# Kernel tuning notes

Measured on AMD Instinct MI355X. Metric: run time of the kernel, lower is better.

Reference implementation:

```python
import jax, jax.numpy as jnp
import numpy as np

ALPHA = 0.2  # LeakyReLU negative slope
NEG_INF = -9e15


def setup_inputs() -> dict:
    key = jax.random.key(0)
    ks = jax.random.split(key, 6)
    B, N, F_in, F_out = 16, 1024, 1024, 512
    x = jax.random.normal(ks[0], (B, N, F_in), dtype=jnp.float32)
    adj = jax.random.randint(ks[1], (B, N, N), 0, 2, dtype=jnp.int32)
    W = jax.random.normal(ks[2], (F_in, F_out), dtype=jnp.float32) * 0.02
    a = jax.random.normal(ks[3], (2 * F_out, 1), dtype=jnp.float32) * 0.02
    fc_w = jax.random.normal(ks[4], (F_out, 2 * F_out), dtype=jnp.float32) * 0.02
    fc_b = jnp.zeros((F_out,), dtype=jnp.float32)
    return {"x": x, "adj": adj, "W": W, "a": a, "fc_w": fc_w, "fc_b": fc_b}


def reference(x, adj, W, a, fc_w, fc_b):
    # h: [B, N, F_out]
    h = jnp.matmul(x, W)
    F_out = W.shape[1]
    # The original builds a_input = concat(h_i, h_j) of shape [B,N,N,2F] and
    # contracts with a. Equivalently (same math, no O(N^2 F) intermediate):
    # e_ij = leakyrelu(h_i . a[:F] + h_j . a[F:])
    a1 = a[:F_out, 0]  # [F_out]
    a2 = a[F_out:, 0]  # [F_out]
    f1 = jnp.einsum('bnf,f->bn', h, a1)  # source term
    f2 = jnp.einsum('bnf,f->bn', h, a2)  # target term
    e = jax.nn.leaky_relu(f1[:, :, None] + f2[:, None, :], negative_slope=ALPHA)  # [B,N,N]
    attention = jnp.where(adj > 0, e, jnp.full_like(e, NEG_INF))
    attention = jax.nn.softmax(attention, axis=2)
    # dropout is identity in eval mode
    agg = jnp.matmul(attention, h)  # [B,N,F_out]
    h_prime = jnp.concatenate([agg, h], axis=2)  # [B,N,2F]
    h_prime = jnp.matmul(h_prime, fc_w.T) + fc_b
    return jax.nn.elu(h_prime)  # concat=True path
```

## Files before the change

### kernel.cpp

```cpp
#include <hip/hip_runtime.h>

#define ALPHA 0.2f

typedef __attribute__((ext_vector_type(8))) short short8;
typedef __attribute__((ext_vector_type(4))) float f32x4;

__device__ __forceinline__ unsigned short f2b(float f) {
  unsigned int u; __builtin_memcpy(&u, &f, 4);
  unsigned int r = (u + 0x7FFFu + ((u >> 16) & 1u)) >> 16;
  return (unsigned short)r;
}
__device__ __forceinline__ float b2f(unsigned short v) {
  unsigned int u = ((unsigned int)v) << 16; float f; __builtin_memcpy(&f, &u, 4); return f;
}
__device__ __forceinline__ void gl_lds16(const unsigned short* g, unsigned short* l) {
  __builtin_amdgcn_global_load_lds((__attribute__((address_space(1))) void*)g,
                                   (__attribute__((address_space(3))) void*)l, 16, 0, 0);
}

__device__ __forceinline__ void cvt8(const float* __restrict__ in, unsigned short* __restrict__ out,
                                     unsigned int gid) {
  float4 v0 = ((const float4*)in)[gid * 2];
  float4 v1 = ((const float4*)in)[gid * 2 + 1];
  alignas(16) unsigned short o[8];
  o[0] = f2b(v0.x); o[1] = f2b(v0.y); o[2] = f2b(v0.z); o[3] = f2b(v0.w);
  o[4] = f2b(v1.x); o[5] = f2b(v1.y); o[6] = f2b(v1.z); o[7] = f2b(v1.w);
  ((uint4*)out)[gid] = *(const uint4*)o;
}

__global__ __launch_bounds__(256) void prep1(const int* __restrict__ adj,
                                             unsigned short* __restrict__ bm16,
                                             const float* __restrict__ x,
                                             unsigned short* __restrict__ xb,
                                             const float* __restrict__ fcw,
                                             unsigned short* __restrict__ fcwb,
                                             const float* __restrict__ W,
                                             unsigned short* __restrict__ Wt) {
  __shared__ alignas(16) unsigned short tile[64][72];
  unsigned int bx = blockIdx.x;
  unsigned int tid = threadIdx.x;
  if (bx < 4096u) {
    unsigned int gid = bx * 256 + tid;
    const int4* a4 = (const int4*)adj;
    int4 v0 = a4[gid * 4 + 0];
    int4 v1 = a4[gid * 4 + 1];
    int4 v2 = a4[gid * 4 + 2];
    int4 v3 = a4[gid * 4 + 3];
    unsigned int bits = 0;
    bits |= (v0.x > 0) << 0;  bits |= (v0.y > 0) << 1;  bits |= (v0.z > 0) << 2;  bits |= (v0.w > 0) << 3;
    bits |= (v1.x > 0) << 4;  bits |= (v1.y > 0) << 5;  bits |= (v1.z > 0) << 6;  bits |= (v1.w > 0) << 7;
    bits |= (v2.x > 0) << 8;  bits |= (v2.y > 0) << 9;  bits |= (v2.z > 0) << 10; bits |= (v2.w > 0) << 11;
    bits |= (v3.x > 0) << 12; bits |= (v3.y > 0) << 13; bits |= (v3.z > 0) << 14; bits |= (v3.w > 0) << 15;
    bm16[gid] = (unsigned short)bits;
  } else if (bx < 12288u) {
    cvt8(x, xb, (bx - 4096u) * 256 + tid);
  } else if (bx < 12544u) {
    cvt8(fcw, fcwb, (bx - 12288u) * 256 + tid);
  } else {
    unsigned int idx = bx - 12544u;
    unsigned int k0 = (idx >> 3) * 64, n0 = (idx & 7) * 64;
    #pragma unroll
    for (int p = 0; p < 4; p++) {
      int r = p * 16 + (tid >> 4);
      int c = (tid & 15) * 4;
      float4 v = *(const float4*)(W + (size_t)(k0 + r) * 512 + n0 + c);
      tile[r][c] = f2b(v.x); tile[r][c + 1] = f2b(v.y);
      tile[r][c + 2] = f2b(v.z); tile[r][c + 3] = f2b(v.w);
    }
    __syncthreads();
    int f = tid >> 2;
    int ic = (tid & 3) * 16;
    alignas(16) unsigned short buf[16];
    #pragma unroll
    for (int k = 0; k < 16; k++) buf[k] = tile[ic + k][f];
    uint4* dst = (uint4*)(Wt + (size_t)(n0 + f) * 1024 + k0 + ic);
    dst[0] = ((const uint4*)buf)[0];
    dst[1] = ((const uint4*)buf)[1];
  }
}

__global__ __launch_bounds__(256) void prep2(const unsigned short* __restrict__ hp,
                                             const float* __restrict__ a,
                                             float* __restrict__ f1, float* __restrict__ f2,
                                             unsigned short* __restrict__ ht) {
  __shared__ alignas(16) unsigned short tile[64][72];
  int bx = blockIdx.x;
  int tid = threadIdx.x;
  if (bx < 4096) {
    int row = bx * 4 + (tid >> 6);
    int lane = tid & 63;
    const unsigned short* hrow = hp + (size_t)row * 1024 + 512;
    uint4 raw = *(const uint4*)(hrow + lane * 8);
    alignas(16) unsigned short hv[8]; __builtin_memcpy(hv, &raw, 16);
    float s1 = 0.f, s2 = 0.f;
    #pragma unroll
    for (int j = 0; j < 8; j++) {
      float hf = b2f(hv[j]);
      s1 += hf * a[lane * 8 + j];
      s2 += hf * a[512 + lane * 8 + j];
    }
    #pragma unroll
    for (int o = 32; o > 0; o >>= 1) { s1 += __shfl_down(s1, o); s2 += __shfl_down(s2, o); }
    if (lane == 0) { f1[row] = s1; f2[row] = s2; }
  } else {
    int idx = bx - 4096;
    int b = idx >> 7;
    int f0 = ((idx >> 4) & 7) * 64;
    int i0 = (idx & 15) * 64;
    #pragma unroll
    for (int p = 0; p < 2; p++) {
      int r = p * 32 + (tid >> 3);
      int c = (tid & 7) * 8;
      uint4 v = *(const uint4*)(hp + (size_t)(b * 1024 + i0 + r) * 1024 + 512 + f0 + c);
      *(uint4*)(&tile[r][c]) = v;
    }
    __syncthreads();
    int f = tid >> 2;
    int ic = (tid & 3) * 16;
    alignas(16) unsigned short buf[16];
    #pragma unroll
    for (int k = 0; k < 16; k++) buf[k] = tile[ic + k][f];
    uint4* dst = (uint4*)(ht + (size_t)(b * 512 + f0 + f) * 1024 + i0 + ic);
    dst[0] = ((const uint4*)buf)[0];
    dst[1] = ((const uint4*)buf)[1];
  }
}

__global__ __launch_bounds__(256) void rowsum_P(const unsigned short* __restrict__ bm16,
                                                const float* __restrict__ f1,
                                                const float* __restrict__ f2,
                                                float* __restrict__ invl,
                                                unsigned short* __restrict__ P) {
  int row = blockIdx.x * 4 + (threadIdx.x >> 6);
  int lane = threadIdx.x & 63;
  int b = row >> 10;
  float f1v = f1[row];
  unsigned int bits = bm16[(size_t)row * 64 + lane];
  const float* f2p = f2 + (b << 10) + lane * 16;
  float4 v0 = ((const float4*)f2p)[0];
  float4 v1 = ((const float4*)f2p)[1];
  float4 v2 = ((const float4*)f2p)[2];
  float4 v3 = ((const float4*)f2p)[3];
  float fv[16] = {v0.x, v0.y, v0.z, v0.w, v1.x, v1.y, v1.z, v1.w,
                  v2.x, v2.y, v2.z, v2.w, v3.x, v3.y, v3.z, v3.w};
  float s = 0.f;
  alignas(16) unsigned short o[16];
  #pragma unroll
  for (int j = 0; j < 16; j++) {
    float p = 0.f;
    if ((bits >> j) & 1u) {
      float z = f1v + fv[j];
      z = z > 0.f ? z : ALPHA * z;
      p = __expf(z);
      s += p;
    }
    o[j] = f2b(p);
  }
  uint4* dst = (uint4*)(P + (size_t)row * 1024 + lane * 16);
  dst[0] = ((const uint4*)o)[0];
  dst[1] = ((const uint4*)o)[1];
  #pragma unroll
  for (int off = 32; off > 0; off >>= 1) s += __shfl_down(s, off);
  if (lane == 0) invl[row] = 1.0f / s;
}

template <int EPI>
__global__ __launch_bounds__(256) void gemm_bt(
    const unsigned short* __restrict__ A, size_t aBS,
    const unsigned short* __restrict__ Bt, size_t bBS,
    int K,
    void* __restrict__ outp, size_t oBS, int ldo, int ocol,
    const float* __restrict__ scale,
    const float* __restrict__ bias) {
  __shared__ alignas(16) unsigned short As[128 * 64];
  __shared__ alignas(16) unsigned short Bs[128 * 64];
  const int tid = threadIdx.x;
  const int lane = tid & 63;
  const int w = tid >> 6;
  const int m0 = blockIdx.x * 128;
  const int n0 = blockIdx.y * 128;
  const int zb = blockIdx.z;
  const unsigned short* Ab = A + (size_t)zb * aBS;
  const unsigned short* Btb = Bt + (size_t)zb * bBS;

  f32x4 acc[4][4];
  #pragma unroll
  for (int i = 0; i < 4; i++)
    #pragma unroll
    for (int j = 0; j < 4; j++)
      #pragma unroll
      for (int r = 0; r < 4; r++) acc[i][j][r] = 0.f;

  const int lr = lane >> 3;
  const int lc = (lane & 7) ^ (lr & 7);
  const unsigned short* ag = Ab + (size_t)(m0 + w * 32 + lr) * K + lc * 8;
  const unsigned short* bg = Btb + (size_t)(n0 + w * 32 + lr) * K + lc * 8;
  unsigned short* asl = As + w * 32 * 64;
  unsigned short* bsl = Bs + w * 32 * 64;

  const int wm = (w & 1) * 64;
  const int wn = (w >> 1) * 64;
  const int row16 = lane & 15;
  const int quad = lane >> 4;
  const int sw = row16 & 7;

  for (int k0 = 0; k0 < K; k0 += 64) {
    __syncthreads();
    #pragma unroll
    for (int t = 0; t < 4; t++) {
      gl_lds16(ag + k0 + (size_t)(t * 8) * K, asl + t * 512);
      gl_lds16(bg + k0 + (size_t)(t * 8) * K, bsl + t * 512);
    }
    __syncthreads();
    short8 af[2][4], bf[2][4];
    #pragma unroll
    for (int s = 0; s < 2; s++) {
      #pragma unroll
      for (int i = 0; i < 4; i++) {
        af[s][i] = *(const short8*)(As + (wm + i * 16 + row16) * 64 + ((s * 4 + quad) ^ sw) * 8);
        bf[s][i] = *(const short8*)(Bs + (wn + i * 16 + row16) * 64 + ((s * 4 + quad) ^ sw) * 8);
      }
    }
    #pragma unroll
    for (int s = 0; s < 2; s++)
      #pragma unroll
      for (int am = 0; am < 4; am++)
        #pragma unroll
        for (int bn = 0; bn < 4; bn++)
          acc[am][bn] = __builtin_amdgcn_mfma_f32_16x16x32_bf16(af[s][am], bf[s][bn], acc[am][bn], 0, 0, 0);
  }

  const int col = lane & 15;
  const int r0 = quad * 4;
  #pragma unroll
  for (int am = 0; am < 4; am++) {
    #pragma unroll
    for (int bn = 0; bn < 4; bn++) {
      #pragma unroll
      for (int r = 0; r < 4; r++) {
        int m = m0 + wm + am * 16 + r0 + r;
        int n = n0 + wn + bn * 16 + col;
        float v = acc[am][bn][r];
        if (EPI == 3) v *= scale[zb * 1024 + m];
        if (EPI == 2) {
          v += bias[n];
          v = v > 0.f ? v : expm1f(v);
          ((float*)outp)[(size_t)m * ldo + n] = v;
        } else {
          ((unsigned short*)outp)[(size_t)zb * oBS + (size_t)m * ldo + ocol + n] = f2b(v);
        }
      }
    }
  }
}

extern "C" void kernel_launch(void* const* d_in, const int* in_sizes, int n_in,
                              void* d_out, int out_size, void* d_ws, size_t ws_size,
                              hipStream_t stream) {
  const float* x   = (const float*)d_in[0];
  const int*   adj = (const int*)d_in[1];
  const float* W   = (const float*)d_in[2];
  const float* a   = (const float*)d_in[3];
  const float* fcw = (const float*)d_in[4];
  const float* fcb = (const float*)d_in[5];
  float* out = (float*)d_out;
  char* ws = (char*)d_ws;

  unsigned short* xb   = (unsigned short*)(ws);
  unsigned short* hp   = (unsigned short*)(ws + 33554432);
  unsigned short* ht   = (unsigned short*)(ws + 67108864);
  unsigned short* Wt   = (unsigned short*)(ws + 83886080);
  unsigned short* fcwb = (unsigned short*)(ws + 84934656);
  float* f1            = (float*)(ws + 85983232);
  float* f2            = (float*)(ws + 86048768);
  float* invl          = (float*)(ws + 86114304);
  unsigned short* bm   = (unsigned short*)(ws + 86179840);
  unsigned short* P = xb;

  prep1<<<12672, 256, 0, stream>>>(adj, bm, x, xb, fcw, fcwb, W, Wt);

  gemm_bt<1><<<dim3(128, 4, 1), 256, 0, stream>>>(xb, 0, Wt, 0, 1024,
                                                  hp, 0, 1024, 512, nullptr, nullptr);
  prep2<<<6144, 256, 0, stream>>>(hp, a, f1, f2, ht);
  rowsum_P<<<4096, 256, 0, stream>>>(bm, f1, f2, invl, P);

  gemm_bt<3><<<dim3(8, 4, 16), 256, 0, stream>>>(P, 1024 * 1024, ht, 512 * 1024, 1024,
                                                 hp, 1024 * 1024, 1024, 0, invl, nullptr);
  gemm_bt<2><<<dim3(128, 4, 1), 256, 0, stream>>>(hp, 0, fcwb, 0, 1024,
                                                  out, 0, 512, 0, nullptr, fcb);
}
```

Measured before the change: 265.8 us.

## Double-buffer GEMM LDS tiles and coalesce adjacency and conversion prep loads

The bf16 GEMM now uses two LDS buffers per operand and issues the next K-tile's global-to-LDS loads before computing on the current tile, with one barrier per iteration instead of two. The goal is to overlap global memory latency with MFMA work. In the prep kernel, adjacency bitmask packing and fp32-to-bf16 conversion are reorganized for coalesced per-lane 16-byte loads, using shuffles to assemble the mask bits. The cost is double the LDS per block (64KB), which may lower occupancy.

```diff
diff --git a/kernel.cpp b/kernel.cpp
--- a/kernel.cpp
+++ b/kernel.cpp
@@ -18,14 +18,13 @@
                                    (__attribute__((address_space(3))) void*)l, 16, 0, 0);
 }
 
-__device__ __forceinline__ void cvt8(const float* __restrict__ in, unsigned short* __restrict__ out,
-                                     unsigned int gid) {
-  float4 v0 = ((const float4*)in)[gid * 2];
-  float4 v1 = ((const float4*)in)[gid * 2 + 1];
-  alignas(16) unsigned short o[8];
-  o[0] = f2b(v0.x); o[1] = f2b(v0.y); o[2] = f2b(v0.z); o[3] = f2b(v0.w);
-  o[4] = f2b(v1.x); o[5] = f2b(v1.y); o[6] = f2b(v1.z); o[7] = f2b(v1.w);
-  ((uint4*)out)[gid] = *(const uint4*)o;
+__device__ __forceinline__ void cvt_f4(const float* __restrict__ in,
+                                       unsigned short* __restrict__ out,
+                                       unsigned int f4idx) {
+  float4 v = ((const float4*)in)[f4idx];
+  alignas(8) unsigned short o[4];
+  o[0] = f2b(v.x); o[1] = f2b(v.y); o[2] = f2b(v.z); o[3] = f2b(v.w);
+  ((uint2*)out)[f4idx] = *(const uint2*)o;
 }
 
 __global__ __launch_bounds__(256) void prep1(const int* __restrict__ adj,
@@ -40,22 +39,30 @@
   unsigned int bx = blockIdx.x;
   unsigned int tid = threadIdx.x;
   if (bx < 4096u) {
-    unsigned int gid = bx * 256 + tid;
-    const int4* a4 = (const int4*)adj;
-    int4 v0 = a4[gid * 4 + 0];
-    int4 v1 = a4[gid * 4 + 1];
-    int4 v2 = a4[gid * 4 + 2];
-    int4 v3 = a4[gid * 4 + 3];
-    unsigned int bits = 0;
-    bits |= (v0.x > 0) << 0;  bits |= (v0.y > 0) << 1;  bits |= (v0.z > 0) << 2;  bits |= (v0.w > 0) << 3;
-    bits |= (v1.x > 0) << 4;  bits |= (v1.y > 0) << 5;  bits |= (v1.z > 0) << 6;  bits |= (v1.w > 0) << 7;
-    bits |= (v2.x > 0) << 8;  bits |= (v2.y > 0) << 9;  bits |= (v2.z > 0) << 10; bits |= (v2.w > 0) << 11;
-    bits |= (v3.x > 0) << 12; bits |= (v3.y > 0) << 13; bits |= (v3.z > 0) << 14; bits |= (v3.w > 0) << 15;
-    bm16[gid] = (unsigned short)bits;
+    unsigned int gw = bx * 4u + (tid >> 6);
+    int lane = tid & 63;
+    const int4* a4 = (const int4*)adj + (size_t)gw * 256;
+    unsigned short* ob = bm16 + (size_t)gw * 64;
+    #pragma unroll
+    for (int t = 0; t < 4; t++) {
+      int4 v = a4[t * 64 + lane];
+      unsigned nib = (unsigned)(v.x > 0) | ((unsigned)(v.y > 0) << 1) |
+                     ((unsigned)(v.z > 0) << 2) | ((unsigned)(v.w > 0) << 3);
+      unsigned n1 = __shfl_down(nib, 1);
+      unsigned n2 = __shfl_down(nib, 2);
+      unsigned n3 = __shfl_down(nib, 3);
+      if ((lane & 3) == 0)
+        ob[t * 16 + (lane >> 2)] =
+            (unsigned short)(nib | (n1 << 4) | (n2 << 8) | (n3 << 12));
+    }
   } else if (bx < 12288u) {
-    cvt8(x, xb, (bx - 4096u) * 256 + tid);
+    unsigned int base = (bx - 4096u) * 512u;
+    cvt_f4(x, xb, base + tid);
+    cvt_f4(x, xb, base + 256u + tid);
   } else if (bx < 12544u) {
-    cvt8(fcw, fcwb, (bx - 12288u) * 256 + tid);
+    unsigned int base = (bx - 12288u) * 512u;
+    cvt_f4(fcw, fcwb, base + tid);
+    cvt_f4(fcw, fcwb, base + 256u + tid);
   } else {
     unsigned int idx = bx - 12544u;
     unsigned int k0 = (idx >> 3) * 64, n0 = (idx & 7) * 64;
@@ -172,8 +179,8 @@
     void* __restrict__ outp, size_t oBS, int ldo, int ocol,
     const float* __restrict__ scale,
     const float* __restrict__ bias) {
-  __shared__ alignas(16) unsigned short As[128 * 64];
-  __shared__ alignas(16) unsigned short Bs[128 * 64];
+  __shared__ alignas(16) unsigned short As[2 * 128 * 64];
+  __shared__ alignas(16) unsigned short Bs[2 * 128 * 64];
   const int tid = threadIdx.x;
   const int lane = tid & 63;
   const int w = tid >> 6;
@@ -195,8 +202,7 @@
   const int lc = (lane & 7) ^ (lr & 7);
   const unsigned short* ag = Ab + (size_t)(m0 + w * 32 + lr) * K + lc * 8;
   const unsigned short* bg = Btb + (size_t)(n0 + w * 32 + lr) * K + lc * 8;
-  unsigned short* asl = As + w * 32 * 64;
-  unsigned short* bsl = Bs + w * 32 * 64;
+  const int sbase = w * 32 * 64;
 
   const int wm = (w & 1) * 64;
   const int wn = (w >> 1) * 64;
@@ -204,21 +210,30 @@
   const int quad = lane >> 4;
   const int sw = row16 & 7;
 
+  #pragma unroll
+  for (int t = 0; t < 4; t++) {
+    gl_lds16(ag + (size_t)(t * 8) * K, As + sbase + t * 512);
+    gl_lds16(bg + (size_t)(t * 8) * K, Bs + sbase + t * 512);
+  }
+  __syncthreads();
+
+  int bufo = 0;
   for (int k0 = 0; k0 < K; k0 += 64) {
-    __syncthreads();
-    #pragma unroll
-    for (int t = 0; t < 4; t++) {
-      gl_lds16(ag + k0 + (size_t)(t * 8) * K, asl + t * 512);
-      gl_lds16(bg + k0 + (size_t)(t * 8) * K, bsl + t * 512);
-    }
-    __syncthreads();
+    const int nbufo = bufo ^ 8192;
+    if (k0 + 64 < K) {
+      #pragma unroll
+      for (int t = 0; t < 4; t++) {
+        gl_lds16(ag + (k0 + 64) + (size_t)(t * 8) * K, As + nbufo + sbase + t * 512);
+        gl_lds16(bg + (k0 + 64) + (size_t)(t * 8) * K, Bs + nbufo + sbase + t * 512);
+      }
+    }
     short8 af[2][4], bf[2][4];
     #pragma unroll
     for (int s = 0; s < 2; s++) {
       #pragma unroll
       for (int i = 0; i < 4; i++) {
-        af[s][i] = *(const short8*)(As + (wm + i * 16 + row16) * 64 + ((s * 4 + quad) ^ sw) * 8);
-        bf[s][i] = *(const short8*)(Bs + (wn + i * 16 + row16) * 64 + ((s * 4 + quad) ^ sw) * 8);
+        af[s][i] = *(const short8*)(As + bufo + (wm + i * 16 + row16) * 64 + ((s * 4 + quad) ^ sw) * 8);
+        bf[s][i] = *(const short8*)(Bs + bufo + (wn + i * 16 + row16) * 64 + ((s * 4 + quad) ^ sw) * 8);
       }
     }
     #pragma unroll
@@ -228,6 +243,8 @@
         #pragma unroll
         for (int bn = 0; bn < 4; bn++)
           acc[am][bn] = __builtin_amdgcn_mfma_f32_16x16x32_bf16(af[s][am], bf[s][bn], acc[am][bn], 0, 0, 0);
+    __syncthreads();
+    bufo = nbufo;
   }
 
   const int col = lane & 15;
```

New measurement: 265.7 us. No clear change (-0.1%).
